# Performance work log

Hardware: AMD Instinct MI355X
Metric: run time of the kernel (lower is better)

## Reference

```python
import jax, jax.numpy as jnp
import numpy as np
from jax import lax

B, U, D = 16, 2048, 512


def setup_inputs() -> dict:
    key = jax.random.key(0)
    ks = jax.random.split(key, 6)
    xs = jax.random.normal(ks[0], (B, U, D), dtype=jnp.float32)
    xlens = jax.random.randint(ks[1], (B,), U // 2, U + 1).astype(jnp.int32)
    ylens = jax.random.randint(ks[2], (B,), 128, 257).astype(jnp.int32)
    # Conv1d(D, D, kernel_size=3, padding=1): weight [O, I, K], bias [O]
    conv_w = jax.random.normal(ks[3], (D, D, 3), dtype=jnp.float32) * (1.0 / np.sqrt(3 * D))
    conv_b = jnp.zeros((D,), dtype=jnp.float32)
    # Linear(D, 1)
    lin_w = jax.random.normal(ks[4], (1, D), dtype=jnp.float32) * (1.0 / np.sqrt(D))
    lin_b = jnp.zeros((1,), dtype=jnp.float32)
    return {"xs": xs, "xlens": xlens, "ylens": ylens,
            "conv_w": conv_w, "conv_b": conv_b, "lin_w": lin_w, "lin_b": lin_b}


def _forward(xs, xlens, ylens, conv_w, conv_b, lin_w, lin_b, u_max):
    # alpha gate: conv1d -> relu -> linear -> sigmoid
    h = lax.conv_general_dilated(xs.transpose(0, 2, 1), conv_w, (1,), ((1, 1),),
                                 dimension_numbers=("NCH", "OIH", "NCH"))
    h = jax.nn.relu(h + conv_b[None, :, None])          # [B, D, U]
    alpha = jax.nn.sigmoid(jnp.einsum("bdu,od->bu", h, lin_w) + lin_b[0])  # [B, U]
    # zero padded positions (positions >= xlen)
    pos = jnp.arange(U)[None, :]
    alpha = jnp.where(pos >= xlens[:, None], 0.0, alpha)
    sum_alpha = alpha.sum(-1)                            # [B]
    beta = sum_alpha / ylens.astype(sum_alpha.dtype) - 1e-4  # [B]

    def step(carry, inp):
        prev_alpha, prev_state = carry                   # [B], [B, D]
        cur_alpha, cur_state = inp                       # [B], [B, D]
        new_alpha = prev_alpha + cur_alpha
        fired = new_alpha >= beta                        # [B]
        left = (beta - prev_alpha)[:, None]
        right = (new_alpha - beta)[:, None]
        integ = prev_state + left * cur_state            # integrated state at fire
        next_alpha = jnp.where(fired, right[:, 0], new_alpha)
        next_state = jnp.where(fired[:, None], right * cur_state, integ)
        next_fired = jnp.where(fired[:, None], integ, jnp.zeros_like(integ))
        return (next_alpha, next_state), next_fired

    init = (jnp.zeros((B,), xs.dtype), jnp.zeros((B, D), xs.dtype))
    _, fired_seq = lax.scan(step, init, (alpha.T, xs.transpose(1, 0, 2)))
    fired_state = fired_seq.transpose(1, 0, 2)           # [B, U, D]

    # stable-move fired frames to the front of each batch row
    marks = jnp.abs(fired_state).sum(-1) != 0.0          # [B, U] bool
    order = jnp.argsort(~marks, axis=1, stable=True)     # fired (False-key) first
    cif_output = jnp.take_along_axis(fired_state, order[:, :, None], axis=1)
    h_cif = cif_output[:, :u_max, :]
    return h_cif, sum_alpha


def reference(xs, xlens, ylens, conv_w, conv_b, lin_w, lin_b):
    u_max = int(jnp.max(ylens))
    return _forward(xs, xlens, ylens, conv_w, conv_b, lin_w, lin_b, u_max)
```

## Files before the change

### kernel.cpp

```cpp
#include <hip/hip_runtime.h>
#include <cstddef>
#include <cstdint>

#define Bb 16
#define Uu 2048
#define Dd 512
#define BU (Bb*Uu)

typedef short bf16x8 __attribute__((ext_vector_type(8)));
typedef float f32x4 __attribute__((ext_vector_type(4)));

#define A_PLANE 2080
#define A_SPLIT 8320
#define A_BYTES 16640
#define B_SLICE 16384
#define B_BASE  16640
#define STEP_BYTES 65536
#define SMEM_BYTES (B_BASE + B_SLICE)

#define WAITVM(N) asm volatile("s_waitcnt vmcnt(" #N ")" ::: "memory")
#define WAITLGKM0 asm volatile("s_waitcnt lgkmcnt(0)" ::: "memory")

__device__ __forceinline__ unsigned short f2bf(float x){
  unsigned int u = __float_as_uint(x);
  u += 0x7fff + ((u >> 16) & 1);
  return (unsigned short)(u >> 16);
}
__device__ __forceinline__ float bf2f(unsigned short b){
  return __uint_as_float(((unsigned int)b) << 16);
}

union U16x8 { unsigned short s[8]; uint4 v; };

__device__ __forceinline__ void split2(float x, unsigned short& h, unsigned short& m){
  h = f2bf(x);
  float r1 = x - bf2f(h);
  m = f2bf(r1);
}

__global__ __launch_bounds__(256) void pack_b_kernel(const float* __restrict__ conv_w,
                                                     char* __restrict__ Bpack){
  int idx = blockIdx.x * 256 + threadIdx.x;
  int n = idx >> 6, cg = idx & 63;
  int chunk = cg >> 2, lg = cg & 3, c0 = cg << 3;
  const float* src = conv_w + (size_t)n * (Dd * 3) + (size_t)c0 * 3;
  float w[24];
  #pragma unroll
  for (int j = 0; j < 24; ++j) w[j] = src[j];
  int cs = n >> 7, cc = n & 127, cgrp = cc >> 4, li = cc & 15;
  char* base = Bpack + (size_t)cs * B_SLICE + cgrp * 2048 + lg * 256 + li * 16;
  #pragma unroll
  for (int tap = 0; tap < 3; ++tap){
    U16x8 H, M;
    #pragma unroll
    for (int j = 0; j < 8; ++j) split2(w[j * 3 + tap], H.s[j], M.s[j]);
    char* dst = base + (size_t)(chunk * 3 + tap) * STEP_BYTES;
    *(uint4*)dst = H.v;
    *(uint4*)(dst + 1024) = M.v;
  }
}

__device__ __forceinline__ void stage_A_direct(char* abuf, const float* __restrict__ xsb,
                                               int u0, int c0, int tid){
  #pragma unroll
  for (int it = 0; it < 3; ++it){
    if (it < 2 || tid < 8){
      int t = (it < 2) ? (tid + it * 256) : (512 + tid);
      int r = t >> 2, lgw = t & 3;
      int uu = u0 - 1 + r;
      float x[8];
      if (uu >= 0 && uu < Uu){
        const float* p = xsb + (size_t)uu * Dd + c0 + lgw * 8;
        float4 a = *(const float4*)p;
        float4 b = *(const float4*)(p + 4);
        x[0]=a.x; x[1]=a.y; x[2]=a.z; x[3]=a.w; x[4]=b.x; x[5]=b.y; x[6]=b.z; x[7]=b.w;
      } else {
        #pragma unroll
        for (int j = 0; j < 8; ++j) x[j] = 0.f;
      }
      U16x8 H, M;
      #pragma unroll
      for (int j = 0; j < 8; ++j) split2(x[j], H.s[j], M.s[j]);
      char* dst = abuf + lgw * A_PLANE + r * 16;
      *(uint4*)(dst)           = H.v;
      *(uint4*)(dst + A_SPLIT) = M.v;
    }
  }
}

__device__ __forceinline__ void gll16(const char* g, char* l){
  __builtin_amdgcn_global_load_lds(
      (const __attribute__((address_space(1))) unsigned int*)g,
      (__attribute__((address_space(3))) unsigned int*)l, 16, 0, 0);
}

__device__ __forceinline__ void stage_slice(char* ldsB, const char* __restrict__ src,
                                            int lane, int wv){
  const char* g = src + wv * 1024 + lane * 16;
  char* l = ldsB + wv * 1024;
  gll16(g, l);
  gll16(g + 4096,  l + 4096);
  gll16(g + 8192,  l + 8192);
  gll16(g + 12288, l + 12288);
}

__device__ __forceinline__ bf16x8 ldfrag(const char* p){
  return __builtin_bit_cast(bf16x8, *(const uint4*)p);
}

__global__ __launch_bounds__(256, 4) void conv_mfma_full_kernel(
    const float* __restrict__ xs, const char* __restrict__ Bpack,
    const float* __restrict__ conv_b, const float* __restrict__ lin_w,
    const int* __restrict__ xlens,
    float* __restrict__ partial)
{
  __shared__ __align__(16) char smem[SMEM_BYTES];
  const int tid = threadIdx.x;
  const int lane = tid & 63, wv = tid >> 6;
  const int wm = wv >> 1;
  const int wn = wv & 1;
  const int ut = blockIdx.x >> 6;
  const int cs = (blockIdx.x >> 4) & 3;
  const int b  = blockIdx.x & 15;
  const int u0 = ut * 128;
  if (u0 >= xlens[b]) return;
  const float* xsb = xs + (size_t)b * Uu * Dd;
  const int li = lane & 15, lg = lane >> 4;

  f32x4 acc[4][4];
  #pragma unroll
  for (int m = 0; m < 4; ++m)
    #pragma unroll
    for (int n = 0; n < 4; ++n){
      f32x4 z = {0.f, 0.f, 0.f, 0.f};
      acc[m][n] = z;
    }

  stage_A_direct(smem, xsb, u0, 0, tid);
  __syncthreads();

  for (int chunk = 0; chunk < 16; ++chunk){
    const bool more = (chunk < 15);
    char* aC = smem;

    bf16x8 a[4][2];
    #pragma unroll
    for (int m = 0; m < 4; ++m){
      const char* ar = aC + lg * A_PLANE + (size_t)(wm * 64 + m * 16 + li) * 16;
      a[m][0] = ldfrag(ar);
      a[m][1] = ldfrag(ar + A_SPLIT);
    }

    #pragma unroll
    for (int tap = 0; tap < 3; ++tap){
      const int p = chunk * 3 + tap;
      const bool apf_now = (tap == 2) && more;

      stage_slice(smem + B_BASE,
                  Bpack + (size_t)p * STEP_BYTES + (size_t)cs * B_SLICE, lane, wv);

      float4 pa0, pa1, pb0, pb1, pe0, pe1;
      int rA = 0, cgA = 0, rE = 0, lgE = 0;
      bool aval = true, eval_ = true;
      if (apf_now){
        const float4 z4 = make_float4(0.f,0.f,0.f,0.f);
        int c0n = (chunk + 1) * 32;
        rA = tid >> 2; cgA = tid & 3;
        int uuA = u0 - 1 + rA;
        aval = (uuA >= 0);
        int uuAc = aval ? uuA : 0;
        const float* pp = xsb + (size_t)uuAc * Dd + c0n + cgA * 8;
        pa0 = *(const float4*)pp;
        pa1 = *(const float4*)(pp + 4);
        if (!aval){ pa0 = z4; pa1 = z4; }
        const float* pq = xsb + (size_t)(u0 + 63 + rA) * Dd + c0n + cgA * 8;
        pb0 = *(const float4*)pq;
        pb1 = *(const float4*)(pq + 4);
        int q = wv * 2 + lane;
        rE = 128 + (q >> 2); lgE = q & 3;
        int uuE = u0 - 1 + rE;
        eval_ = (uuE < Uu);
        int uuEc = eval_ ? uuE : (Uu - 1);
        pe0 = z4; pe1 = z4;
        if (lane < 2){
          const float* pr = xsb + (size_t)uuEc * Dd + c0n + lgE * 8;
          pe0 = *(const float4*)pr;
          pe1 = *(const float4*)(pr + 4);
        }
        if (!eval_){ pe0 = z4; pe1 = z4; }
        __builtin_amdgcn_sched_barrier(0);
      }

      if (apf_now) { WAITVM(6); } else { WAITVM(0); }
      __builtin_amdgcn_sched_barrier(0);
      __builtin_amdgcn_s_barrier();

      __builtin_amdgcn_s_setprio(1);
      const char* bbase = smem + B_BASE;
      #pragma unroll
      for (int n = 0; n < 4; ++n){
        const char* br = bbase + (size_t)(wn * 4 + n) * 2048 + lg * 256 + li * 16;
        bf16x8 bh = ldfrag(br);
        bf16x8 bm = ldfrag(br + 1024);
        #pragma unroll
        for (int m = 0; m < 4; ++m) acc[m][n] = __builtin_amdgcn_mfma_f32_16x16x32_bf16(a[m][0], bh, acc[m][n], 0, 0, 0);
        #pragma unroll
        for (int m = 0; m < 4; ++m) acc[m][n] = __builtin_amdgcn_mfma_f32_16x16x32_bf16(a[m][1], bh, acc[m][n], 0, 0, 0);
        #pragma unroll
        for (int m = 0; m < 4; ++m) acc[m][n] = __builtin_amdgcn_mfma_f32_16x16x32_bf16(a[m][0], bm, acc[m][n], 0, 0, 0);
        #pragma unroll
        for (int m = 0; m < 4; ++m) acc[m][n] = __builtin_amdgcn_mfma_f32_16x16x32_bf16(a[m][1], bm, acc[m][n], 0, 0, 0);
      }
      __builtin_amdgcn_s_setprio(0);

      if (tap < 2){
        #pragma unroll
        for (int m = 0; m < 4; ++m){
          const char* ar = aC + lg * A_PLANE + (size_t)(wm * 64 + m * 16 + li + tap + 1) * 16;
          a[m][0] = ldfrag(ar);
          a[m][1] = ldfrag(ar + A_SPLIT);
        }
      }

      if (apf_now){
        WAITVM(0);
        __builtin_amdgcn_sched_barrier(0);
        __builtin_amdgcn_s_barrier();
        U16x8 H, M;
        float x[8];
        x[0]=pa0.x; x[1]=pa0.y; x[2]=pa0.z; x[3]=pa0.w;
        x[4]=pa1.x; x[5]=pa1.y; x[6]=pa1.z; x[7]=pa1.w;
        #pragma unroll
        for (int jj = 0; jj < 8; ++jj) split2(x[jj], H.s[jj], M.s[jj]);
        char* dA = aC + cgA * A_PLANE + rA * 16;
        *(uint4*)(dA)           = H.v;
        *(uint4*)(dA + A_SPLIT) = M.v;
        x[0]=pb0.x; x[1]=pb0.y; x[2]=pb0.z; x[3]=pb0.w;
        x[4]=pb1.x; x[5]=pb1.y; x[6]=pb1.z; x[7]=pb1.w;
        #pragma unroll
        for (int jj = 0; jj < 8; ++jj) split2(x[jj], H.s[jj], M.s[jj]);
        char* dB = aC + cgA * A_PLANE + (64 + rA) * 16;
        *(uint4*)(dB)           = H.v;
        *(uint4*)(dB + A_SPLIT) = M.v;
        if (lane < 2){
          float y[8];
          y[0]=pe0.x; y[1]=pe0.y; y[2]=pe0.z; y[3]=pe0.w;
          y[4]=pe1.x; y[5]=pe1.y; y[6]=pe1.z; y[7]=pe1.w;
          #pragma unroll
          for (int jj = 0; jj < 8; ++jj) split2(y[jj], H.s[jj], M.s[jj]);
          char* dE = aC + lgE * A_PLANE + rE * 16;
          *(uint4*)(dE)           = H.v;
          *(uint4*)(dE + A_SPLIT) = M.v;
        }
        WAITLGKM0;
        __builtin_amdgcn_sched_barrier(0);
      }
      __builtin_amdgcn_s_barrier();
    }
  }

  __syncthreads();
  float* pbuf = (float*)smem;
  #pragma unroll
  for (int m = 0; m < 4; ++m){
    float s0 = 0.f, s1 = 0.f, s2 = 0.f, s3 = 0.f;
    #pragma unroll
    for (int n = 0; n < 4; ++n){
      int col = cs * 128 + wn * 64 + n * 16 + li;
      float cb = conv_b[col], lw = lin_w[col];
      f32x4 v = acc[m][n];
      float h;
      h = v[0] + cb; h = h > 0.f ? h : 0.f; s0 += h * lw;
      h = v[1] + cb; h = h > 0.f ? h : 0.f; s1 += h * lw;
      h = v[2] + cb; h = h > 0.f ? h : 0.f; s2 += h * lw;
      h = v[3] + cb; h = h > 0.f ? h : 0.f; s3 += h * lw;
    }
    #pragma unroll
    for (int msk = 1; msk < 16; msk <<= 1){
      s0 += __shfl_xor(s0, msk); s1 += __shfl_xor(s1, msk);
      s2 += __shfl_xor(s2, msk); s3 += __shfl_xor(s3, msk);
    }
    if (li == 0){
      int fr = wm * 64 + m * 16 + lg * 4;
      pbuf[(fr + 0) * 2 + wn] = s0;
      pbuf[(fr + 1) * 2 + wn] = s1;
      pbuf[(fr + 2) * 2 + wn] = s2;
      pbuf[(fr + 3) * 2 + wn] = s3;
    }
  }
  __syncthreads();
  if (tid < 128){
    float pv = pbuf[tid * 2] + pbuf[tid * 2 + 1];
    partial[(size_t)cs * BU + (size_t)b * Uu + u0 + tid] = pv;
  }
}

__global__ __launch_bounds__(64) void scan_kernel(
    const float* __restrict__ partial, const float* __restrict__ lin_b,
    const int* __restrict__ xlens, const int* __restrict__ ylens,
    float* __restrict__ wA, float* __restrict__ wB,
    int* __restrict__ fire_pos, int* __restrict__ nf,
    float* __restrict__ out_sum)
{
  __shared__ float salpha[Uu];
  int b = blockIdx.x;
  int lane = threadIdx.x;
  int xl = xlens[b];
  int xce = (xl + 63) & ~63;
  float lb = lin_b[0];

  float sum = 0.f;
  for (int u0 = 0; u0 < xce; u0 += 64){
    int u = u0 + lane;
    size_t ix = (size_t)b * Uu + u;
    float v = lb + partial[ix] + partial[BU + ix] + partial[2 * BU + ix] + partial[3 * BU + ix];
    float a = 1.f / (1.f + expf(-v));
    if (u >= xl) a = 0.f;
    salpha[u] = a;
    sum += a;
  }
  #pragma unroll
  for (int m = 1; m < 64; m <<= 1) sum += __shfl_xor(sum, m);
  float sa = sum;
  float beta = sa / (float)ylens[b] - 1e-4f;
  if (lane == 0) out_sum[b] = sa;

  float prev = 0.f;
  int cnt = 0;
  for (int u0 = 0; u0 < Uu; u0 += 64) {
    if (u0 >= xl) break;
    float val = salpha[u0 + lane];
    float mywa = 0.f, mywb = 0.f;
    #pragma unroll
    for (int i = 0; i < 64; ++i) {
      float a_cur = __builtin_bit_cast(float,
          __builtin_amdgcn_readlane(__builtin_bit_cast(int, val), i));
      float nw = prev + a_cur;
      float left = beta - prev;
      float right = nw - beta;
      bool fired = nw >= beta;
      if (lane == i) { mywa = left; mywb = right; }
      if (fired) {
        if (lane == 0) fire_pos[(b << 11) + cnt] = u0 + i;
        ++cnt;
      }
      prev = fired ? right : nw;
    }
    wA[(size_t)b * Uu + u0 + lane] = mywa;
    wB[(size_t)b * Uu + u0 + lane] = mywb;
  }
  if (lane == 0) nf[b] = cnt;
}

__global__ __launch_bounds__(512) void gather_kernel(
    const float* __restrict__ xs, const float* __restrict__ wA, const float* __restrict__ wB,
    const int* __restrict__ fire_pos, const int* __restrict__ nf,
    float* __restrict__ out, int umax)
{
  int t = blockIdx.x, b = blockIdx.y;
  int tid = threadIdx.x;
  float* o = out + ((size_t)b * umax + t) * Dd;
  int n = nf[b];
  if (t >= n) { o[tid] = 0.f; return; }
  int start = (t == 0) ? 0 : fire_pos[(b << 11) + t - 1];
  int end = fire_pos[(b << 11) + t];
  const float* xb = xs + (size_t)b * Uu * Dd;
  float acc = 0.f;
  for (int u = start; u <= end; ++u) {
    float w = (t > 0 && u == start) ? wB[(size_t)b * Uu + u] : wA[(size_t)b * Uu + u];
    acc += w * xb[(size_t)u * Dd + tid];
  }
  o[tid] = acc;
}

extern "C" void kernel_launch(void* const* d_in, const int* in_sizes, int n_in,
                              void* d_out, int out_size, void* d_ws, size_t ws_size,
                              hipStream_t stream) {
  const float* xs     = (const float*)d_in[0];
  const int*   xlens  = (const int*)d_in[1];
  const int*   ylens  = (const int*)d_in[2];
  const float* conv_w = (const float*)d_in[3];
  const float* conv_b = (const float*)d_in[4];
  const float* lin_w  = (const float*)d_in[5];
  const float* lin_b  = (const float*)d_in[6];
  float* out = (float*)d_out;
  int umax = (out_size - Bb) / (Bb * Dd);

  char* ws = (char*)d_ws;
  char*  Bpack    = ws;
  float* partial  = (float*)(ws + 48 * (size_t)STEP_BYTES);
  float* wAv      = partial + 4 * BU;
  float* wBv      = wAv + BU;
  int*   fire_pos = (int*)(wBv + BU);
  int*   nf       = (int*)(fire_pos + BU);

  pack_b_kernel<<<(512 * 64) / 256, 256, 0, stream>>>(conv_w, Bpack);
  conv_mfma_full_kernel<<<1024, 256, 0, stream>>>(xs, Bpack, conv_b, lin_w, xlens, partial);
  scan_kernel<<<Bb, 64, 0, stream>>>(partial, lin_b, xlens, ylens, wAv, wBv, fire_pos, nf,
                                     out + (size_t)Bb * umax * Dd);
  if (umax > 0)
    gather_kernel<<<dim3(umax, Bb), 512, 0, stream>>>(xs, wAv, wBv, fire_pos, nf, out, umax);
}
```

Baseline: 314.9 us.

## Split B weight slice into halves and ping-pong loads across MFMA phases

Splits each per-step B weight slice into two halves with a repacked layout. While one half is consumed by MFMAs, the other half for the current or next step is in flight via global_load_lds, replacing the single load-then-wait per tap. This hides weight-load latency behind compute and keeps the same LDS footprint. In exchange it adds an extra barrier per tap and relies on more delicate vmcnt accounting, including the A-prefetch waits.

```diff
diff --git a/kernel.cpp b/kernel.cpp
--- a/kernel.cpp
+++ b/kernel.cpp
@@ -13,10 +13,11 @@
 #define A_PLANE 2080
 #define A_SPLIT 8320
 #define A_BYTES 16640
+#define B_HALF 8192
 #define B_SLICE 16384
 #define B_BASE  16640
 #define STEP_BYTES 65536
-#define SMEM_BYTES (B_BASE + B_SLICE)
+#define SMEM_BYTES (B_BASE + 2*B_HALF)
 
 #define WAITVM(N) asm volatile("s_waitcnt vmcnt(" #N ")" ::: "memory")
 #define WAITLGKM0 asm volatile("s_waitcnt lgkmcnt(0)" ::: "memory")
@@ -47,8 +48,9 @@
   float w[24];
   #pragma unroll
   for (int j = 0; j < 24; ++j) w[j] = src[j];
-  int cs = n >> 7, cc = n & 127, cgrp = cc >> 4, li = cc & 15;
-  char* base = Bpack + (size_t)cs * B_SLICE + cgrp * 2048 + lg * 256 + li * 16;
+  int cs = n >> 7, cc = n & 127, c = cc >> 4, li = cc & 15;
+  int h = (c & 3) >> 1, local = (c >> 2) * 2 + (c & 1);
+  char* base = Bpack + (size_t)cs * B_SLICE + h * B_HALF + local * 2048 + lg * 256 + li * 16;
   #pragma unroll
   for (int tap = 0; tap < 3; ++tap){
     U16x8 H, M;
@@ -94,14 +96,12 @@
       (__attribute__((address_space(3))) unsigned int*)l, 16, 0, 0);
 }
 
-__device__ __forceinline__ void stage_slice(char* ldsB, const char* __restrict__ src,
-                                            int lane, int wv){
+__device__ __forceinline__ void stage_half(char* ldsB, const char* __restrict__ src,
+                                           int lane, int wv){
   const char* g = src + wv * 1024 + lane * 16;
   char* l = ldsB + wv * 1024;
   gll16(g, l);
-  gll16(g + 4096,  l + 4096);
-  gll16(g + 8192,  l + 8192);
-  gll16(g + 12288, l + 12288);
+  gll16(g + 4096, l + 4096);
 }
 
 __device__ __forceinline__ bf16x8 ldfrag(const char* p){
@@ -137,6 +137,7 @@
     }
 
   stage_A_direct(smem, xsb, u0, 0, tid);
+  stage_half(smem + B_BASE, Bpack + (size_t)cs * B_SLICE, lane, wv);
   __syncthreads();
 
   for (int chunk = 0; chunk < 16; ++chunk){
@@ -155,9 +156,9 @@
     for (int tap = 0; tap < 3; ++tap){
       const int p = chunk * 3 + tap;
       const bool apf_now = (tap == 2) && more;
-
-      stage_slice(smem + B_BASE,
-                  Bpack + (size_t)p * STEP_BYTES + (size_t)cs * B_SLICE, lane, wv);
+      const char* stepb = Bpack + (size_t)p * STEP_BYTES + (size_t)cs * B_SLICE;
+
+      stage_half(smem + B_BASE + B_HALF, stepb + B_HALF, lane, wv);
 
       float4 pa0, pa1, pb0, pb1, pe0, pe1;
       int rA = 0, cgA = 0, rE = 0, lgE = 0;
@@ -191,15 +192,42 @@
         __builtin_amdgcn_sched_barrier(0);
       }
 
-      if (apf_now) { WAITVM(6); } else { WAITVM(0); }
+      if (apf_now) { WAITVM(8); } else { WAITVM(2); }
       __builtin_amdgcn_sched_barrier(0);
       __builtin_amdgcn_s_barrier();
 
       __builtin_amdgcn_s_setprio(1);
-      const char* bbase = smem + B_BASE;
       #pragma unroll
-      for (int n = 0; n < 4; ++n){
-        const char* br = bbase + (size_t)(wn * 4 + n) * 2048 + lg * 256 + li * 16;
+      for (int n2 = 0; n2 < 2; ++n2){
+        const char* br = smem + B_BASE + (size_t)(wn * 2 + n2) * 2048 + lg * 256 + li * 16;
+        bf16x8 bh = ldfrag(br);
+        bf16x8 bm = ldfrag(br + 1024);
+        #pragma unroll
+        for (int m = 0; m < 4; ++m) acc[m][n2] = __builtin_amdgcn_mfma_f32_16x16x32_bf16(a[m][0], bh, acc[m][n2], 0, 0, 0);
+        #pragma unroll
+        for (int m = 0; m < 4; ++m) acc[m][n2] = __builtin_amdgcn_mfma_f32_16x16x32_bf16(a[m][1], bh, acc[m][n2], 0, 0, 0);
+        #pragma unroll
+        for (int m = 0; m < 4; ++m) acc[m][n2] = __builtin_amdgcn_mfma_f32_16x16x32_bf16(a[m][0], bm, acc[m][n2], 0, 0, 0);
+        #pragma unroll
+        for (int m = 0; m < 4; ++m) acc[m][n2] = __builtin_amdgcn_mfma_f32_16x16x32_bf16(a[m][1], bm, acc[m][n2], 0, 0, 0);
+      }
+      __builtin_amdgcn_s_setprio(0);
+      __builtin_amdgcn_s_barrier();
+
+      if (p < 47)
+        stage_half(smem + B_BASE, Bpack + (size_t)(p + 1) * STEP_BYTES + (size_t)cs * B_SLICE,
+                   lane, wv);
+      if (p == 47)       { WAITVM(0); }
+      else if (apf_now)  { WAITVM(8); }
+      else               { WAITVM(2); }
+      __builtin_amdgcn_sched_barrier(0);
+      __builtin_amdgcn_s_barrier();
+
+      __builtin_amdgcn_s_setprio(1);
+      #pragma unroll
+      for (int n2 = 0; n2 < 2; ++n2){
+        const int n = 2 + n2;
+        const char* br = smem + B_BASE + B_HALF + (size_t)(wn * 2 + n2) * 2048 + lg * 256 + li * 16;
         bf16x8 bh = ldfrag(br);
         bf16x8 bm = ldfrag(br + 1024);
         #pragma unroll
@@ -223,9 +251,8 @@
       }
 
       if (apf_now){
-        WAITVM(0);
+        WAITVM(2);
         __builtin_amdgcn_sched_barrier(0);
-        __builtin_amdgcn_s_barrier();
         U16x8 H, M;
         float x[8];
         x[0]=pa0.x; x[1]=pa0.y; x[2]=pa0.z; x[3]=pa0.w;
```

Result: faster. 291.6 us (-7.4%).
